# Kernel optimization log

Measured on AMD Instinct MI355X. Metric: run time of the kernel, lower is better.

Reference implementation:

```python
import jax, jax.numpy as jnp
import numpy as np

N_ITERS = 1000   # n_iters default
LR = 0.1         # SGD lr default (schedule_lr=False -> constant lr)
EPS = 1e-8       # eps in LogMagTargetFrequencyLoss


def setup_inputs() -> dict:
    key = jax.random.key(0)
    k1, k2 = jax.random.split(key)
    # random log-magnitude target in dB (scaled to plausible dB range)
    target_dB = jax.random.normal(k1, (512,), dtype=jnp.float32) * 6.0
    # matches torch.rand(1, 16, 6) init of self.coefs / self.sos
    sos_init = jax.random.uniform(k2, (1, 16, 6), dtype=jnp.float32)
    return {"target_dB": target_dB, "sos_init": sos_init}


def _log_mag_loss(sos, target):
    """LogMagTargetFrequencyLoss: MSE between 20*log10|H(e^jw)| of the SOS
    cascade and the target dB response. sos: (1,16,6); target: (1,N)."""
    n = target.shape[-1]
    w = jnp.linspace(0.0, jnp.pi, n)                      # frequency grid (N,)
    zm = jnp.exp(-1j * w.astype(jnp.complex64))            # z^-1 on unit circle
    powers = jnp.stack([jnp.ones_like(zm), zm, zm * zm])   # (3, N): [1, z^-1, z^-2]
    b = sos[..., :3].astype(jnp.complex64)                 # (1,16,3)
    a = sos[..., 3:].astype(jnp.complex64)                 # (1,16,3)
    num = jnp.einsum('bsc,cn->bsn', b, powers)             # (1,16,N)
    den = jnp.einsum('bsc,cn->bsn', a, powers)             # (1,16,N)
    h = jnp.prod(num / den, axis=1)                        # cascade product -> (1,N)
    mag = 20.0 * jnp.log10(jnp.abs(h) + EPS)
    return jnp.mean((mag - target) ** 2)


def reference(target_dB, sos_init):
    target = target_dB.reshape(1, -1)
    grad_fn = jax.grad(_log_mag_loss)

    def step(sos, _):
        g = grad_fn(sos, target)
        return sos - LR * g, None   # plain SGD, constant lr (schedule_lr=False)

    sos, _ = jax.lax.scan(step, sos_init, None, length=N_ITERS)
    # pole_zero=False: out_sos aliases self.sos, so the returned tensor is the
    # post-step (final optimized) coefficients.
    return sos
```

## Files before the change

### kernel.cpp

```cpp
#include <hip/hip_runtime.h>
#include <math.h>

#define NITER 1000
#define LRATE 0.1f

typedef unsigned int v2u __attribute__((ext_vector_type(2)));

__device__ __forceinline__ float rcpf(float x) { return __builtin_amdgcn_rcpf(x); }

__device__ __forceinline__ float readlane_f(float v, int l) {
    return __int_as_float(__builtin_amdgcn_readlane(__float_as_int(v), l));
}

template<int CTRL>
__device__ __forceinline__ float dpp_mov(float v) {
    return __int_as_float(__builtin_amdgcn_update_dpp(0, __float_as_int(v), CTRL, 0xF, 0xF, true));
}

__device__ __forceinline__ int lane_id() {
    return __builtin_amdgcn_mbcnt_hi(~0u, __builtin_amdgcn_mbcnt_lo(~0u, 0u));
}

__device__ __forceinline__ void swap16(float& x, float& y) {
#if __has_builtin(__builtin_amdgcn_permlane16_swap)
    v2u r = __builtin_amdgcn_permlane16_swap(__float_as_uint(x), __float_as_uint(y), false, false);
    x = __uint_as_float(r[0]);
    y = __uint_as_float(r[1]);
#else
    const bool up = lane_id() & 16;
    const float send = up ? x : y;
    const float recv = __shfl_xor(send, 16);
    x = up ? recv : x;
    y = up ? y : recv;
#endif
}

__device__ __forceinline__ void swap32(float& x, float& y) {
#if __has_builtin(__builtin_amdgcn_permlane32_swap)
    v2u r = __builtin_amdgcn_permlane32_swap(__float_as_uint(x), __float_as_uint(y), false, false);
    x = __uint_as_float(r[0]);
    y = __uint_as_float(r[1]);
#else
    const bool up = lane_id() & 32;
    const float send = up ? x : y;
    const float recv = __shfl_xor(send, 32);
    x = up ? recv : x;
    y = up ? y : recv;
#endif
}

__global__ __launch_bounds__(512, 1)
void sgd_filter_design_kernel(const float* __restrict__ target,
                              const float* __restrict__ sos_init,
                              float* __restrict__ out)
{
    const int t = threadIdx.x;
    const int w = t >> 6;
    const int L = t & 63;

    __shared__ __align__(16) float wq[8][576];
    __shared__ __align__(16) float Kbuf[576];

    const float PI = 3.14159265358979323846f;
    float C1[8], C2[8];
    #pragma unroll
    for (int f = 0; f < 8; ++f) {
        const int n = 8 * L + f;
        const float wr = PI * (float)n / 511.0f;
        const float c1 = cosf(wr);
        C1[f] = c1;
        C2[f] = 2.0f * c1 * c1 - 1.0f;
    }

    const float mKt = -0.03392925639869154f * target[t];
    const int kaddr = 8 * (t >> 3) + 4 * (t >> 5) + (t & 7);
    const int sw = 8 * L + 4 * (L >> 2);

    const int col = ((L & 16) >> 1) | ((L & 32) >> 3) | ((L & 1) << 1) | ((L & 2) >> 1);
    const bool up1 = L & 1, up2 = L & 2;

    float v0 = 0.0f;
    if (col < 12) v0 = sos_init[12 * w + col];
    float b0A = readlane_f(v0, 0);
    float b1A = readlane_f(v0, 2);
    float b2A = readlane_f(v0, 1);
    float a0A = readlane_f(v0, 3);
    float a1A = readlane_f(v0, 32);
    float a2A = readlane_f(v0, 34);
    float b0B = readlane_f(v0, 33);
    float b1B = readlane_f(v0, 35);
    float b2B = readlane_f(v0, 16);
    float a0B = readlane_f(v0, 18);
    float a1B = readlane_f(v0, 17);
    float a2B = readlane_f(v0, 19);

    for (int it = 0; it < NITER; ++it) {
        const float PA0 = fmaf(b0A, b0A, fmaf(b1A, b1A, b2A * b2A));
        const float PA1 = 2.0f * b1A * (b0A + b2A);
        const float PA2 = 2.0f * b0A * b2A;
        const float QA0 = fmaf(a0A, a0A, fmaf(a1A, a1A, a2A * a2A));
        const float QA1 = 2.0f * a1A * (a0A + a2A);
        const float QA2 = 2.0f * a0A * a2A;
        const float PB0 = fmaf(b0B, b0B, fmaf(b1B, b1B, b2B * b2B));
        const float PB1 = 2.0f * b1B * (b0B + b2B);
        const float PB2 = 2.0f * b0B * b2B;
        const float QB0 = fmaf(a0B, a0B, fmaf(a1B, a1B, a2B * a2B));
        const float QB1 = 2.0f * a1B * (a0B + a2B);
        const float QB2 = 2.0f * a0B * a2B;

        float imnA[8], imdA[8], imnB[8], imdB[8], qs[8];
        #pragma unroll
        for (int f = 0; f < 8; ++f) {
            float mnA = fmaf(PA2, C2[f], fmaf(PA1, C1[f], PA0));
            float mdA = fmaf(QA2, C2[f], fmaf(QA1, C1[f], QA0));
            float mnB = fmaf(PB2, C2[f], fmaf(PB1, C1[f], PB0));
            float mdB = fmaf(QB2, C2[f], fmaf(QB1, C1[f], QB0));
            mnA = fmaxf(mnA, 1e-18f);
            mdA = fmaxf(mdA, 1e-18f);
            mnB = fmaxf(mnB, 1e-18f);
            mdB = fmaxf(mdB, 1e-18f);
            const float rA = rcpf(mnA * mdA);
            const float rB = rcpf(mnB * mdB);
            imnA[f] = rA * mdA; imdA[f] = rA * mnA;
            imnB[f] = rB * mdB; imdB[f] = rB * mnB;
            qs[f] = (mnA * imdA[f]) * (mnB * imdB[f]);
        }
        {
            const float4 q0 = {qs[0], qs[1], qs[2], qs[3]};
            const float4 q1 = {qs[4], qs[5], qs[6], qs[7]};
            *reinterpret_cast<float4*>(&wq[w][sw])     = q0;
            *reinterpret_cast<float4*>(&wq[w][sw + 4]) = q1;
        }
        __syncthreads();

        {
            float p0 = wq[0][kaddr], p1 = wq[1][kaddr];
            float p2 = wq[2][kaddr], p3 = wq[3][kaddr];
            const float p4 = wq[4][kaddr], p5 = wq[5][kaddr];
            const float p6 = wq[6][kaddr], p7 = wq[7][kaddr];
            p0 *= p4; p1 *= p5; p2 *= p6; p3 *= p7;
            p0 *= p2; p1 *= p3;
            p0 *= p1;
            Kbuf[kaddr] = fmaf(__log2f(p0), 0.10213724040f, mKt);
        }
        __syncthreads();

        const float4 k0 = *reinterpret_cast<const float4*>(&Kbuf[sw]);
        const float4 k1 = *reinterpret_cast<const float4*>(&Kbuf[sw + 4]);
        const float Kf[8] = {k0.x, k0.y, k0.z, k0.w, k1.x, k1.y, k1.z, k1.w};

        float SA0, SA1, SA2, TA0, TA1, TA2;
        float SB0, SB1, SB2, TB0, TB1, TB2;
        #pragma unroll
        for (int f = 0; f < 8; ++f) {
            const float EA = Kf[f] * imnA[f];
            const float FA = Kf[f] * imdA[f];
            const float EB = Kf[f] * imnB[f];
            const float FB = Kf[f] * imdB[f];
            if (f == 0) {
                SA0 = EA;          TA0 = FA;
                SA1 = EA * C1[f];  TA1 = FA * C1[f];
                SA2 = EA * C2[f];  TA2 = FA * C2[f];
                SB0 = EB;          TB0 = FB;
                SB1 = EB * C1[f];  TB1 = FB * C1[f];
                SB2 = EB * C2[f];  TB2 = FB * C2[f];
            } else {
                SA0 += EA;                    TA0 += FA;
                SA1 = fmaf(EA, C1[f], SA1);   TA1 = fmaf(FA, C1[f], TA1);
                SA2 = fmaf(EA, C2[f], SA2);   TA2 = fmaf(FA, C2[f], TA2);
                SB0 += EB;                    TB0 += FB;
                SB1 = fmaf(EB, C1[f], SB1);   TB1 = fmaf(FB, C1[f], TB1);
                SB2 = fmaf(EB, C2[f], SB2);   TB2 = fmaf(FB, C2[f], TB2);
            }
        }
        const float g12[12] = {SA0, SA1, SA2, TA0, TA1, TA2,
                               SB0, SB1, SB2, TB0, TB1, TB2};

        float r8v[8];
        #pragma unroll
        for (int i = 0; i < 8; ++i) {
            float x = g12[i];
            float y = (i + 8 < 12) ? g12[i + 8] : 0.0f;
            swap16(x, y);
            r8v[i] = x + y;
        }
        float r4v[4];
        #pragma unroll
        for (int i = 0; i < 4; ++i) {
            float x = r8v[i], y = r8v[i + 4];
            swap32(x, y);
            r4v[i] = x + y;
        }
        float r2v[2];
        #pragma unroll
        for (int i = 0; i < 2; ++i) {
            const float x = r4v[i], y = r4v[i + 2];
            const float P = up1 ? y : x, Q = up1 ? x : y;
            r2v[i] = P + dpp_mov<0xB1>(Q);
        }
        float r1v;
        {
            const float x = r2v[0], y = r2v[1];
            const float P = up2 ? y : x, Q = up2 ? x : y;
            r1v = P + dpp_mov<0x4E>(Q);
        }
        r1v += dpp_mov<0x128>(r1v);
        r1v += __shfl_xor(r1v, 4);

        const float sSA0 = readlane_f(r1v, 0);
        const float sSA1 = readlane_f(r1v, 2);
        const float sSA2 = readlane_f(r1v, 1);
        const float sTA0 = readlane_f(r1v, 3);
        const float sTA1 = readlane_f(r1v, 32);
        const float sTA2 = readlane_f(r1v, 34);
        const float sSB0 = readlane_f(r1v, 33);
        const float sSB1 = readlane_f(r1v, 35);
        const float sSB2 = readlane_f(r1v, 16);
        const float sTB0 = readlane_f(r1v, 18);
        const float sTB1 = readlane_f(r1v, 17);
        const float sTB2 = readlane_f(r1v, 19);

        const float gb0A = fmaf(b0A, sSA0, fmaf(b1A, sSA1, b2A * sSA2));
        const float gb1A = fmaf(b0A + b2A, sSA1, b1A * sSA0);
        const float gb2A = fmaf(b0A, sSA2, fmaf(b1A, sSA1, b2A * sSA0));
        const float ga0A = fmaf(a0A, sTA0, fmaf(a1A, sTA1, a2A * sTA2));
        const float ga1A = fmaf(a0A + a2A, sTA1, a1A * sTA0);
        const float ga2A = fmaf(a0A, sTA2, fmaf(a1A, sTA1, a2A * sTA0));
        const float gb0B = fmaf(b0B, sSB0, fmaf(b1B, sSB1, b2B * sSB2));
        const float gb1B = fmaf(b0B + b2B, sSB1, b1B * sSB0);
        const float gb2B = fmaf(b0B, sSB2, fmaf(b1B, sSB1, b2B * sSB0));
        const float ga0B = fmaf(a0B, sTB0, fmaf(a1B, sTB1, a2B * sTB2));
        const float ga1B = fmaf(a0B + a2B, sTB1, a1B * sTB0);
        const float ga2B = fmaf(a0B, sTB2, fmaf(a1B, sTB1, a2B * sTB0));

        b0A = fmaf(-LRATE, gb0A, b0A);
        b1A = fmaf(-LRATE, gb1A, b1A);
        b2A = fmaf(-LRATE, gb2A, b2A);
        a0A = fmaf( LRATE, ga0A, a0A);
        a1A = fmaf( LRATE, ga1A, a1A);
        a2A = fmaf( LRATE, ga2A, a2A);
        b0B = fmaf(-LRATE, gb0B, b0B);
        b1B = fmaf(-LRATE, gb1B, b1B);
        b2B = fmaf(-LRATE, gb2B, b2B);
        a0B = fmaf( LRATE, ga0B, a0B);
        a1B = fmaf( LRATE, ga1B, a1B);
        a2B = fmaf( LRATE, ga2B, a2B);
    }

    if (L == 0) {
        out[12 * w + 0]  = b0A;
        out[12 * w + 1]  = b1A;
        out[12 * w + 2]  = b2A;
        out[12 * w + 3]  = a0A;
        out[12 * w + 4]  = a1A;
        out[12 * w + 5]  = a2A;
        out[12 * w + 6]  = b0B;
        out[12 * w + 7]  = b1B;
        out[12 * w + 8]  = b2B;
        out[12 * w + 9]  = a0B;
        out[12 * w + 10] = a1B;
        out[12 * w + 11] = a2B;
    }
}

extern "C" void kernel_launch(void* const* d_in, const int* in_sizes, int n_in,
                              void* d_out, int out_size, void* d_ws, size_t ws_size,
                              hipStream_t stream) {
    const float* target   = (const float*)d_in[0];
    const float* sos_init = (const float*)d_in[1];
    float* out = (float*)d_out;
    hipLaunchKernelGGL(sgd_filter_design_kernel, dim3(1), dim3(512), 0, stream,
                       target, sos_init, out);
}
```

Baseline: 1.529 ms.

## Replace product-reduction staging with LDS atomic log-sum accumulation and double buffering

Each lane now adds log2 of its per-frequency magnitude ratio into a double-buffered LDS accumulator with atomicAdd, replacing the store-all/multiply-reduce/log stage. The barrier for that separate reduction pass is gone, and the buffer for the next iteration is re-seeded with the target term. The cost is 8 log2 evaluations per lane and contended LDS float atomics, where 8 waves hit the same addresses each iteration, plus a barrier at the end of the loop. Summing logs also changes floating-point rounding relative to multiplying products.

```diff
diff --git a/kernel.cpp b/kernel.cpp
--- a/kernel.cpp
+++ b/kernel.cpp
@@ -3,6 +3,8 @@
 
 #define NITER 1000
 #define LRATE 0.1f
+#define KLOG 0.10213724040f
+#define IINIT_SCALE -0.332192809488736f
 
 typedef unsigned int v2u __attribute__((ext_vector_type(2)));
 
@@ -58,8 +60,7 @@
     const int w = t >> 6;
     const int L = t & 63;
 
-    __shared__ __align__(16) float wq[8][576];
-    __shared__ __align__(16) float Kbuf[576];
+    __shared__ float Kacc[2][576];
 
     const float PI = 3.14159265358979323846f;
     float C1[8], C2[8];
@@ -72,9 +73,11 @@
         C2[f] = 2.0f * c1 * c1 - 1.0f;
     }
 
-    const float mKt = -0.03392925639869154f * target[t];
-    const int kaddr = 8 * (t >> 3) + 4 * (t >> 5) + (t & 7);
-    const int sw = 8 * L + 4 * (L >> 2);
+    const float Iinit = IINIT_SCALE * target[t];
+    const int kinit = 9 * (t >> 3) + (t & 7);
+    Kacc[0][kinit] = Iinit;
+
+    const int kbase = 9 * L;
 
     const int col = ((L & 16) >> 1) | ((L & 32) >> 3) | ((L & 1) << 1) | ((L & 2) >> 1);
     const bool up1 = L & 1, up2 = L & 2;
@@ -94,21 +97,24 @@
     float a1B = readlane_f(v0, 17);
     float a2B = readlane_f(v0, 19);
 
+    __syncthreads();
+
+    int cur = 0;
     for (int it = 0; it < NITER; ++it) {
         const float PA0 = fmaf(b0A, b0A, fmaf(b1A, b1A, b2A * b2A));
-        const float PA1 = 2.0f * b1A * (b0A + b2A);
-        const float PA2 = 2.0f * b0A * b2A;
+        float PA1 = b1A * (b0A + b2A); PA1 += PA1;
+        float PA2 = b0A * b2A;         PA2 += PA2;
         const float QA0 = fmaf(a0A, a0A, fmaf(a1A, a1A, a2A * a2A));
-        const float QA1 = 2.0f * a1A * (a0A + a2A);
-        const float QA2 = 2.0f * a0A * a2A;
+        float QA1 = a1A * (a0A + a2A); QA1 += QA1;
+        float QA2 = a0A * a2A;         QA2 += QA2;
         const float PB0 = fmaf(b0B, b0B, fmaf(b1B, b1B, b2B * b2B));
-        const float PB1 = 2.0f * b1B * (b0B + b2B);
-        const float PB2 = 2.0f * b0B * b2B;
+        float PB1 = b1B * (b0B + b2B); PB1 += PB1;
+        float PB2 = b0B * b2B;         PB2 += PB2;
         const float QB0 = fmaf(a0B, a0B, fmaf(a1B, a1B, a2B * a2B));
-        const float QB1 = 2.0f * a1B * (a0B + a2B);
-        const float QB2 = 2.0f * a0B * a2B;
-
-        float imnA[8], imdA[8], imnB[8], imdB[8], qs[8];
+        float QB1 = a1B * (a0B + a2B); QB1 += QB1;
+        float QB2 = a0B * a2B;         QB2 += QB2;
+
+        float imnA[8], imdA[8], imnB[8], imdB[8];
         #pragma unroll
         for (int f = 0; f < 8; ++f) {
             float mnA = fmaf(PA2, C2[f], fmaf(PA1, C1[f], PA0));
@@ -123,31 +129,15 @@
             const float rB = rcpf(mnB * mdB);
             imnA[f] = rA * mdA; imdA[f] = rA * mnA;
             imnB[f] = rB * mdB; imdB[f] = rB * mnB;
-            qs[f] = (mnA * imdA[f]) * (mnB * imdB[f]);
-        }
-        {
-            const float4 q0 = {qs[0], qs[1], qs[2], qs[3]};
-            const float4 q1 = {qs[4], qs[5], qs[6], qs[7]};
-            *reinterpret_cast<float4*>(&wq[w][sw])     = q0;
-            *reinterpret_cast<float4*>(&wq[w][sw + 4]) = q1;
+            const float qAB = (mnA * imdA[f]) * (mnB * imdB[f]);
+            atomicAdd(&Kacc[cur][kbase + f], __log2f(qAB));
         }
         __syncthreads();
 
-        {
-            float p0 = wq[0][kaddr], p1 = wq[1][kaddr];
-            float p2 = wq[2][kaddr], p3 = wq[3][kaddr];
-            const float p4 = wq[4][kaddr], p5 = wq[5][kaddr];
-            const float p6 = wq[6][kaddr], p7 = wq[7][kaddr];
-            p0 *= p4; p1 *= p5; p2 *= p6; p3 *= p7;
-            p0 *= p2; p1 *= p3;
-            p0 *= p1;
-            Kbuf[kaddr] = fmaf(__log2f(p0), 0.10213724040f, mKt);
-        }
-        __syncthreads();
-
-        const float4 k0 = *reinterpret_cast<const float4*>(&Kbuf[sw]);
-        const float4 k1 = *reinterpret_cast<const float4*>(&Kbuf[sw + 4]);
-        const float Kf[8] = {k0.x, k0.y, k0.z, k0.w, k1.x, k1.y, k1.z, k1.w};
+        float Kf[8];
+        #pragma unroll
+        for (int f = 0; f < 8; ++f) Kf[f] = KLOG * Kacc[cur][kbase + f];
+        Kacc[cur ^ 1][kinit] = Iinit;
 
         float SA0, SA1, SA2, TA0, TA1, TA2;
         float SB0, SB1, SB2, TB0, TB1, TB2;
@@ -245,6 +235,9 @@
         a0B = fmaf( LRATE, ga0B, a0B);
         a1B = fmaf( LRATE, ga1B, a1B);
         a2B = fmaf( LRATE, ga2B, a2B);
+
+        __syncthreads();
+        cur ^= 1;
     }
 
     if (L == 0) {
```

New measurement: 6.103 ms. +299.2%, slower.
